# Performance work log

Measured on AMD Instinct MI355X. Metric: run time of the kernel, lower is better.

The kernel has to match this reference:

```python
import jax, jax.numpy as jnp
from jax import lax
import numpy as np

S, D, L, H, C = 128, 3, 16, 512, 10
B, T = 32, 16384


def setup_inputs() -> dict:
    key = jax.random.key(0)
    ks = jax.random.split(key, 6)
    x = jax.random.normal(ks[0], (B, D, T), dtype=jnp.float32)
    shapelets = jax.random.normal(ks[1], (S, 1, D, L), dtype=jnp.float32)  # OIHW, one per shapelet
    W1 = jax.random.normal(ks[2], (H, S), dtype=jnp.float32) * (1.0 / np.sqrt(S))
    b1 = jnp.zeros((H,), dtype=jnp.float32)
    W2 = jax.random.normal(ks[3], (C, H), dtype=jnp.float32) * (1.0 / np.sqrt(H))
    b2 = jnp.zeros((C,), dtype=jnp.float32)
    return {"x": x, "shapelets": shapelets, "W1": W1, "b1": b1, "W2": W2, "b2": b2}


def reference(x, shapelets, W1, b1, W2, b2):
    # x: [B, D, T] -> [B, 1, D, T]; kernels slide only over time (full-height conv).
    x4 = x[:, None, :, :]
    dn = ("NCHW", "OIHW", "NCHW")
    ones_k = jnp.ones((1, 1, shapelets.shape[2], shapelets.shape[3]), dtype=x.dtype)
    # ||window||^2 per sliding window: [B, 1, 1, Tout]
    window_square = lax.conv_general_dilated(x4 * x4, ones_k, (1, 1), "VALID", dimension_numbers=dn)
    # all cross-correlations in one grouped conv: [B, S, 1, Tout]
    cross_corr = lax.conv_general_dilated(x4, shapelets, (1, 1), "VALID", dimension_numbers=dn)
    shapelet_square = jnp.sum(shapelets * shapelets, axis=(1, 2, 3))  # [S]
    # squared distance per (shapelet, window), min-reduced over windows
    dist = window_square + shapelet_square[None, :, None, None] - 2.0 * cross_corr  # [B, S, 1, Tout]
    distance = jnp.min(dist, axis=(2, 3))  # [B, S]
    h = jax.nn.relu(distance @ W1.T + b1)
    classification = h @ W2.T + b2
    return (distance, classification)
```

## Files before the change

kernel.cpp:

```cpp
#include <hip/hip_runtime.h>

#define Bn 32
#define Tn 16384
#define Ln 16
#define Sn 128
#define Hn 512
#define Cn 10
#define Kn 48
#define TOUT 16369
#define CH 1024
#define NCH 16
#define XBP 8224

typedef short  s16x8  __attribute__((ext_vector_type(8)));
typedef float  f32x16 __attribute__((ext_vector_type(16)));

static __device__ __forceinline__ unsigned short f2bf(float f) {
    union { float f; unsigned int u; } v; v.f = f;
    unsigned int r = v.u + 0x7FFF + ((v.u >> 16) & 1);
    return (unsigned short)(r >> 16);
}
static __device__ __forceinline__ float bf2f(unsigned short b) {
    union { unsigned int u; float f; } v; v.u = ((unsigned int)b) << 16;
    return v.f;
}
static __device__ __forceinline__ unsigned int pk(float a, float b) {
    return (unsigned int)f2bf(a) | ((unsigned int)f2bf(b) << 16);
}
static __device__ __forceinline__ unsigned int pk2(unsigned short a, unsigned short b) {
    return (unsigned int)a | ((unsigned int)b << 16);
}
static __device__ __forceinline__ s16x8 mk_a(unsigned int d0, unsigned int d1,
                                             unsigned int d2, unsigned int d3) {
    union { unsigned int u[4]; s16x8 v; } t;
    t.u[0] = d0; t.u[1] = d1; t.u[2] = d2; t.u[3] = d3;
    return t.v;
}
static __device__ __forceinline__ s16x8 mk_a4(uint4 t) {
    union { uint4 u; s16x8 v; } c; c.u = t; return c.v;
}

__global__ __launch_bounds__(256) void prep_kernel(const float* __restrict__ x,
                                                   const float* __restrict__ sh,
                                                   const float* __restrict__ b2,
                                                   unsigned int* __restrict__ shb,
                                                   float* __restrict__ shsq_g,
                                                   float* __restrict__ wsqT,
                                                   unsigned int* __restrict__ xbf,
                                                   float* __restrict__ out) {
    const int tid = threadIdx.x;
    if (blockIdx.x == 0) {
        if (tid < 128) {
            const float4* r4 = (const float4*)(sh + tid * Kn);
            float v[48]; float q = 0.f;
            #pragma unroll
            for (int c = 0; c < 12; ++c) {
                const float4 t = r4[c];
                v[4*c] = t.x; v[4*c+1] = t.y; v[4*c+2] = t.z; v[4*c+3] = t.w;
                q = fmaf(t.x, t.x, q); q = fmaf(t.y, t.y, q);
                q = fmaf(t.z, t.z, q); q = fmaf(t.w, t.w, q);
            }
            shsq_g[tid] = q;
            uint4* dst = (uint4*)(shb + tid * 24);
            #pragma unroll
            for (int c = 0; c < 6; ++c) {
                uint4 o;
                o.x = pk(-2.f*v[8*c  ], -2.f*v[8*c+1]);
                o.y = pk(-2.f*v[8*c+2], -2.f*v[8*c+3]);
                o.z = pk(-2.f*v[8*c+4], -2.f*v[8*c+5]);
                o.w = pk(-2.f*v[8*c+6], -2.f*v[8*c+7]);
                dst[c] = o;
            }
        } else if (tid < 224) {
            const int r = tid - 128;
            uint4* d = (uint4*)(xbf + r * XBP + 8192);
            const uint4 z = {0u, 0u, 0u, 0u};
            #pragma unroll
            for (int q = 0; q < 8; ++q) d[q] = z;
        } else {
            const int k0 = (tid - 224) * 10;
            #pragma unroll
            for (int c = 0; c < Cn; ++c) out[Bn * Sn + k0 + c] = b2[c];
        }
        return;
    }
    const int bid = blockIdx.x - 1;
    const int b   = bid >> 4;
    const int t0  = ((bid & 15) << 10) + 4 * tid;
    float q[4] = {0.f, 0.f, 0.f, 0.f};
    #pragma unroll
    for (int ch = 0; ch < 3; ++ch) {
        const float* xs = x + (b * 3 + ch) * Tn + t0;
        float wv[20];
        if (t0 + 20 <= Tn) {
            const float4* x4 = (const float4*)xs;
            #pragma unroll
            for (int c = 0; c < 5; ++c) {
                const float4 t = x4[c];
                wv[4*c] = t.x; wv[4*c+1] = t.y; wv[4*c+2] = t.z; wv[4*c+3] = t.w;
            }
        } else {
            #pragma unroll
            for (int k = 0; k < 20; ++k) wv[k] = (t0 + k < Tn) ? xs[k] : 0.f;
        }
        float s = 0.f;
        #pragma unroll
        for (int l = 0; l < 16; ++l) s = fmaf(wv[l], wv[l], s);
        q[0] += s;
        #pragma unroll
        for (int j = 1; j < 4; ++j) {
            s = s - wv[j-1]*wv[j-1] + wv[j+15]*wv[j+15];
            q[j] += s;
        }
        uint2 o = { pk(wv[0], wv[1]), pk(wv[2], wv[3]) };
        *(uint2*)(xbf + (b * 3 + ch) * XBP + (t0 >> 1)) = o;
    }
    const int r0 = t0 & 15, col = t0 >> 4;
    float* wrow = wsqT + b * 16384 + col;
    #pragma unroll
    for (int c = 0; c < 4; ++c)
        wrow[(r0 + c) * 1024] = (t0 + c >= TOUT) ? 1e30f : q[c];
}

__global__ __launch_bounds__(256, 3) void dist_kernel(const unsigned int* __restrict__ shb,
                                                      const float* __restrict__ shsq_g,
                                                      const float* __restrict__ wsqT,
                                                      const unsigned int* __restrict__ xbf,
                                                      float* __restrict__ partial) {
    __shared__ float wavemin[4 * 64];

    const int tid   = threadIdx.x;
    const int b     = blockIdx.x >> 5;
    const int rem   = blockIdx.x & 31;
    const int chunk = rem >> 1;
    const int half  = rem & 1;
    const int tb    = chunk * CH;
    const int lane  = tid & 63;
    const int w     = tid >> 6;
    const int n     = lane & 31;
    const int h     = lane >> 5;

    s16x8 bfr[3][2], b4[2];
    #pragma unroll
    for (int st = 0; st < 2; ++st) {
        const int s = half * 64 + st * 32 + n;
        const uint4* base = (const uint4*)(shb + s * 24);
        #pragma unroll
        for (int kk = 0; kk < 3; ++kk) {
            const uint4 t = base[kk * 2 + h];
            bfr[kk][st] = mk_a(t.x, t.y, t.z, t.w);
        }
        const float q = shsq_g[s];
        const unsigned short qh = f2bf(q);
        const unsigned short ql = f2bf(q - bf2f(qh));
        b4[st] = h ? mk_a(0u, 0u, 0u, 0u)
                   : mk_a(0x3F803F80u, pk2(qh, ql), 0u, 0u);
    }

    unsigned int u[3][8];
    {
        const int D0 = (tb >> 1) + 4 * (w & 1) + ((w >> 1) << 8) + 8 * n + 4 * h;
        #pragma unroll
        for (int ch = 0; ch < 3; ++ch) {
            const unsigned int* xr = xbf + (b * 3 + ch) * XBP + D0;
            const uint4 lo = *(const uint4*)(xr);
            const uint4 hi = *(const uint4*)(xr + 4);
            u[ch][0] = lo.x; u[ch][1] = lo.y; u[ch][2] = lo.z; u[ch][3] = lo.w;
            u[ch][4] = hi.x; u[ch][5] = hi.y; u[ch][6] = hi.z; u[ch][7] = hi.w;
        }
    }

    float mcol[2] = {1e30f, 1e30f};
    const f32x16 zero16 = {0.f, 0.f, 0.f, 0.f, 0.f, 0.f, 0.f, 0.f,
                           0.f, 0.f, 0.f, 0.f, 0.f, 0.f, 0.f, 0.f};
    const int   base_t = 8 * (w & 1) + ((w >> 1) << 9);
    const float* wbase = wsqT + b * 16384 + (tb >> 4) + n;

    #pragma unroll
    for (int rr = 0; rr < 8; ++rr) {
        const int i = base_t + rr;
        s16x8 a[3];
        #pragma unroll
        for (int ch = 0; ch < 3; ++ch) {
            if ((rr & 1) == 0) {
                a[ch] = mk_a(u[ch][rr/2], u[ch][rr/2+1], u[ch][rr/2+2], u[ch][rr/2+3]);
            } else {
                unsigned int d[4];
                #pragma unroll
                for (int k = 0; k < 4; ++k)
                    d[k] = (u[ch][rr/2 + k] >> 16) | (u[ch][rr/2 + k + 1] << 16);
                a[ch] = mk_a(d[0], d[1], d[2], d[3]);
            }
        }
        const float wv = wbase[(i & 15) * 1024 + ((i >> 9) << 5)];
        const unsigned short wh = f2bf(wv);
        const unsigned short wl = f2bf(wv - bf2f(wh));
        const s16x8 a4 = h ? mk_a(0u, 0u, 0u, 0u)
                           : mk_a(pk2(wh, wl), 0x3F803F80u, 0u, 0u);

        #pragma unroll
        for (int st = 0; st < 2; ++st) {
            f32x16 acc;
            acc = __builtin_amdgcn_mfma_f32_32x32x16_bf16(a[0], bfr[0][st], zero16, 0, 0, 0);
            acc = __builtin_amdgcn_mfma_f32_32x32x16_bf16(a[1], bfr[1][st], acc, 0, 0, 0);
            acc = __builtin_amdgcn_mfma_f32_32x32x16_bf16(a[2], bfr[2][st], acc, 0, 0, 0);
            acc = __builtin_amdgcn_mfma_f32_32x32x16_bf16(a4,   b4[st],    acc, 0, 0, 0);
            #pragma unroll
            for (int reg = 0; reg < 16; reg += 2)
                mcol[st] = fminf(fminf(mcol[st], acc[reg]), acc[reg + 1]);
        }
    }

    #pragma unroll
    for (int st = 0; st < 2; ++st) {
        float mm = mcol[st];
        mm = fminf(mm, __shfl_xor(mm, 32, 64));
        if (h == 0) wavemin[w * 64 + st * 32 + n] = mm;
    }
    __syncthreads();
    if (tid < 64) {
        const float mm = fminf(fminf(wavemin[tid], wavemin[64 + tid]),
                               fminf(wavemin[128 + tid], wavemin[192 + tid]));
        partial[(b * NCH + chunk) * Sn + half * 64 + tid] = mm;
    }
}

__global__ __launch_bounds__(512) void mlp_kernel(const float* __restrict__ partial,
                                                  const float* __restrict__ W1,
                                                  const float* __restrict__ b1,
                                                  const float* __restrict__ W2,
                                                  float* __restrict__ out) {
    __shared__ float pmin[4][Sn];
    __shared__ float db[Sn];
    __shared__ float hb[128];
    __shared__ float part[Cn][32];
    const int b = blockIdx.x >> 2, g = blockIdx.x & 3, tid = threadIdx.x;

    {
        const int s = tid & 127, cg = tid >> 7;
        const float* pp = partial + (b * NCH + cg * 4) * Sn + s;
        float m = pp[0];
        #pragma unroll
        for (int c = 1; c < 4; ++c) m = fminf(m, pp[c * Sn]);
        pmin[cg][s] = m;
    }
    __syncthreads();
    if (tid < Sn) {
        const float m = fminf(fminf(pmin[0][tid], pmin[1][tid]),
                              fminf(pmin[2][tid], pmin[3][tid]));
        db[tid] = m;
        if (g == 0) out[b * Sn + tid] = m;
    }
    __syncthreads();

    if (tid < 128) {
        const int hrow = g * 128 + tid;
        float a = b1[hrow];
        const float4* w1r = (const float4*)(W1 + hrow * Sn);
        const float4* dbv = (const float4*)db;
        #pragma unroll
        for (int i = 0; i < Sn / 4; ++i) {
            const float4 wv = w1r[i];
            const float4 dv = dbv[i];
            a = fmaf(dv.x, wv.x, a); a = fmaf(dv.y, wv.y, a);
            a = fmaf(dv.z, wv.z, a); a = fmaf(dv.w, wv.w, a);
        }
        hb[tid] = fmaxf(a, 0.0f);
    }
    __syncthreads();

    if (tid < Cn * 32) {
        const int c = tid >> 5, p = tid & 31;
        float acc = 0.f;
        #pragma unroll
        for (int k = 0; k < 4; ++k)
            acc = fmaf(hb[p + 32 * k], W2[c * Hn + g * 128 + p + 32 * k], acc);
        part[c][p] = acc;
    }
    __syncthreads();
    if (tid < Cn) {
        float acc = 0.f;
        #pragma unroll
        for (int p = 0; p < 32; ++p) acc += part[tid][p];
        atomicAdd(&out[Bn * Sn + b * Cn + tid], acc);
    }
}

extern "C" void kernel_launch(void* const* d_in, const int* in_sizes, int n_in,
                              void* d_out, int out_size, void* d_ws, size_t ws_size,
                              hipStream_t stream) {
    const float* x  = (const float*)d_in[0];
    const float* sh = (const float*)d_in[1];
    const float* W1 = (const float*)d_in[2];
    const float* b1 = (const float*)d_in[3];
    const float* W2 = (const float*)d_in[4];
    const float* b2 = (const float*)d_in[5];
    float* out = (float*)d_out;

    char* wsb = (char*)d_ws;
    float*        partial = (float*)wsb;
    unsigned int* shb     = (unsigned int*)(wsb + 262144);
    float*        shsq_g  = (float*)(wsb + 274432);
    float*        wsqT    = (float*)(wsb + 278528);
    unsigned int* xbf     = (unsigned int*)(wsb + 2375680);

    prep_kernel<<<513, 256, 0, stream>>>(x, sh, b2, shb, shsq_g, wsqT, xbf, out);
    dist_kernel<<<Bn * NCH * 2, 256, 0, stream>>>(shb, shsq_g, wsqT, xbf, partial);
    mlp_kernel<<<Bn * 4, 512, 0, stream>>>(partial, W1, b1, W2, out);
}
```

Measured before the change: 97.78 us.

## Fuse prep kernel into distance kernel and drop MLP atomics

Removes the separate prep kernel. The distance kernel now reads fp32 x and the shapelets directly, converts them to bf16, and computes the sliding window squared norms and shapelet norms in registers. This cuts one launch and the round trip through the bf16/transposed workspace buffers, at the cost of redundant shapelet conversion per block and extra per-thread arithmetic. The MLP kernel now runs one block per batch over all 512 hidden units, adding b2 itself and writing the output directly instead of using atomicAdd.

```diff
diff --git a/kernel.cpp b/kernel.cpp
--- a/kernel.cpp
+++ b/kernel.cpp
@@ -10,7 +10,6 @@
 #define TOUT 16369
 #define CH 1024
 #define NCH 16
-#define XBP 8224
 
 typedef short  s16x8  __attribute__((ext_vector_type(8)));
 typedef float  f32x16 __attribute__((ext_vector_type(16)));
@@ -36,96 +35,9 @@
     t.u[0] = d0; t.u[1] = d1; t.u[2] = d2; t.u[3] = d3;
     return t.v;
 }
-static __device__ __forceinline__ s16x8 mk_a4(uint4 t) {
-    union { uint4 u; s16x8 v; } c; c.u = t; return c.v;
-}
-
-__global__ __launch_bounds__(256) void prep_kernel(const float* __restrict__ x,
-                                                   const float* __restrict__ sh,
-                                                   const float* __restrict__ b2,
-                                                   unsigned int* __restrict__ shb,
-                                                   float* __restrict__ shsq_g,
-                                                   float* __restrict__ wsqT,
-                                                   unsigned int* __restrict__ xbf,
-                                                   float* __restrict__ out) {
-    const int tid = threadIdx.x;
-    if (blockIdx.x == 0) {
-        if (tid < 128) {
-            const float4* r4 = (const float4*)(sh + tid * Kn);
-            float v[48]; float q = 0.f;
-            #pragma unroll
-            for (int c = 0; c < 12; ++c) {
-                const float4 t = r4[c];
-                v[4*c] = t.x; v[4*c+1] = t.y; v[4*c+2] = t.z; v[4*c+3] = t.w;
-                q = fmaf(t.x, t.x, q); q = fmaf(t.y, t.y, q);
-                q = fmaf(t.z, t.z, q); q = fmaf(t.w, t.w, q);
-            }
-            shsq_g[tid] = q;
-            uint4* dst = (uint4*)(shb + tid * 24);
-            #pragma unroll
-            for (int c = 0; c < 6; ++c) {
-                uint4 o;
-                o.x = pk(-2.f*v[8*c  ], -2.f*v[8*c+1]);
-                o.y = pk(-2.f*v[8*c+2], -2.f*v[8*c+3]);
-                o.z = pk(-2.f*v[8*c+4], -2.f*v[8*c+5]);
-                o.w = pk(-2.f*v[8*c+6], -2.f*v[8*c+7]);
-                dst[c] = o;
-            }
-        } else if (tid < 224) {
-            const int r = tid - 128;
-            uint4* d = (uint4*)(xbf + r * XBP + 8192);
-            const uint4 z = {0u, 0u, 0u, 0u};
-            #pragma unroll
-            for (int q = 0; q < 8; ++q) d[q] = z;
-        } else {
-            const int k0 = (tid - 224) * 10;
-            #pragma unroll
-            for (int c = 0; c < Cn; ++c) out[Bn * Sn + k0 + c] = b2[c];
-        }
-        return;
-    }
-    const int bid = blockIdx.x - 1;
-    const int b   = bid >> 4;
-    const int t0  = ((bid & 15) << 10) + 4 * tid;
-    float q[4] = {0.f, 0.f, 0.f, 0.f};
-    #pragma unroll
-    for (int ch = 0; ch < 3; ++ch) {
-        const float* xs = x + (b * 3 + ch) * Tn + t0;
-        float wv[20];
-        if (t0 + 20 <= Tn) {
-            const float4* x4 = (const float4*)xs;
-            #pragma unroll
-            for (int c = 0; c < 5; ++c) {
-                const float4 t = x4[c];
-                wv[4*c] = t.x; wv[4*c+1] = t.y; wv[4*c+2] = t.z; wv[4*c+3] = t.w;
-            }
-        } else {
-            #pragma unroll
-            for (int k = 0; k < 20; ++k) wv[k] = (t0 + k < Tn) ? xs[k] : 0.f;
-        }
-        float s = 0.f;
-        #pragma unroll
-        for (int l = 0; l < 16; ++l) s = fmaf(wv[l], wv[l], s);
-        q[0] += s;
-        #pragma unroll
-        for (int j = 1; j < 4; ++j) {
-            s = s - wv[j-1]*wv[j-1] + wv[j+15]*wv[j+15];
-            q[j] += s;
-        }
-        uint2 o = { pk(wv[0], wv[1]), pk(wv[2], wv[3]) };
-        *(uint2*)(xbf + (b * 3 + ch) * XBP + (t0 >> 1)) = o;
-    }
-    const int r0 = t0 & 15, col = t0 >> 4;
-    float* wrow = wsqT + b * 16384 + col;
-    #pragma unroll
-    for (int c = 0; c < 4; ++c)
-        wrow[(r0 + c) * 1024] = (t0 + c >= TOUT) ? 1e30f : q[c];
-}
-
-__global__ __launch_bounds__(256, 3) void dist_kernel(const unsigned int* __restrict__ shb,
-                                                      const float* __restrict__ shsq_g,
-                                                      const float* __restrict__ wsqT,
-                                                      const unsigned int* __restrict__ xbf,
+
+__global__ __launch_bounds__(256, 3) void dist_kernel(const float* __restrict__ x,
+                                                      const float* __restrict__ sh,
                                                       float* __restrict__ partial) {
     __shared__ float wavemin[4 * 64];
 
@@ -144,41 +56,79 @@
     #pragma unroll
     for (int st = 0; st < 2; ++st) {
         const int s = half * 64 + st * 32 + n;
-        const uint4* base = (const uint4*)(shb + s * 24);
+        const float4* row4 = (const float4*)(sh + s * Kn);
+        float q = 0.f;
         #pragma unroll
         for (int kk = 0; kk < 3; ++kk) {
-            const uint4 t = base[kk * 2 + h];
-            bfr[kk][st] = mk_a(t.x, t.y, t.z, t.w);
-        }
-        const float q = shsq_g[s];
+            const float4 v0 = row4[kk * 4 + 0];
+            const float4 v1 = row4[kk * 4 + 1];
+            const float4 v2 = row4[kk * 4 + 2];
+            const float4 v3 = row4[kk * 4 + 3];
+            q = fmaf(v0.x, v0.x, q); q = fmaf(v0.y, v0.y, q);
+            q = fmaf(v0.z, v0.z, q); q = fmaf(v0.w, v0.w, q);
+            q = fmaf(v1.x, v1.x, q); q = fmaf(v1.y, v1.y, q);
+            q = fmaf(v1.z, v1.z, q); q = fmaf(v1.w, v1.w, q);
+            q = fmaf(v2.x, v2.x, q); q = fmaf(v2.y, v2.y, q);
+            q = fmaf(v2.z, v2.z, q); q = fmaf(v2.w, v2.w, q);
+            q = fmaf(v3.x, v3.x, q); q = fmaf(v3.y, v3.y, q);
+            q = fmaf(v3.z, v3.z, q); q = fmaf(v3.w, v3.w, q);
+            const float4 pa = h ? v2 : v0;
+            const float4 pb = h ? v3 : v1;
+            bfr[kk][st] = mk_a(pk(-2.f * pa.x, -2.f * pa.y),
+                               pk(-2.f * pa.z, -2.f * pa.w),
+                               pk(-2.f * pb.x, -2.f * pb.y),
+                               pk(-2.f * pb.z, -2.f * pb.w));
+        }
         const unsigned short qh = f2bf(q);
         const unsigned short ql = f2bf(q - bf2f(qh));
         b4[st] = h ? mk_a(0u, 0u, 0u, 0u)
                    : mk_a(0x3F803F80u, pk2(qh, ql), 0u, 0u);
     }
 
+    const int t0 = tb + 8 * (w & 1) + ((w >> 1) << 9) + 16 * n + 8 * h;
     unsigned int u[3][8];
-    {
-        const int D0 = (tb >> 1) + 4 * (w & 1) + ((w >> 1) << 8) + 8 * n + 4 * h;
-        #pragma unroll
-        for (int ch = 0; ch < 3; ++ch) {
-            const unsigned int* xr = xbf + (b * 3 + ch) * XBP + D0;
-            const uint4 lo = *(const uint4*)(xr);
-            const uint4 hi = *(const uint4*)(xr + 4);
-            u[ch][0] = lo.x; u[ch][1] = lo.y; u[ch][2] = lo.z; u[ch][3] = lo.w;
-            u[ch][4] = hi.x; u[ch][5] = hi.y; u[ch][6] = hi.z; u[ch][7] = hi.w;
-        }
+    float q8[8] = {0.f, 0.f, 0.f, 0.f, 0.f, 0.f, 0.f, 0.f};
+    #pragma unroll
+    for (int ch = 0; ch < 3; ++ch) {
+        const float* xs = x + (b * 3 + ch) * Tn + t0;
+        float wv[24];
+        if (t0 + 24 <= Tn) {
+            const float4* x4 = (const float4*)xs;
+            #pragma unroll
+            for (int c = 0; c < 6; ++c) {
+                const float4 t = x4[c];
+                wv[4*c] = t.x; wv[4*c+1] = t.y; wv[4*c+2] = t.z; wv[4*c+3] = t.w;
+            }
+        } else {
+            #pragma unroll
+            for (int k = 0; k < 24; ++k) wv[k] = (t0 + k < Tn) ? xs[k] : 0.f;
+        }
+        #pragma unroll
+        for (int e = 0; e < 8; ++e) u[ch][e] = pk(wv[2*e], wv[2*e+1]);
+        float s = 0.f;
+        #pragma unroll
+        for (int l = 0; l < 16; ++l) s = fmaf(wv[l], wv[l], s);
+        q8[0] += s;
+        #pragma unroll
+        for (int j = 1; j < 8; ++j) {
+            s = s - wv[j-1] * wv[j-1] + wv[j+15] * wv[j+15];
+            q8[j] += s;
+        }
+    }
+    unsigned int wqp[8];
+    #pragma unroll
+    for (int rr = 0; rr < 8; ++rr) {
+        const float qv = (t0 + rr >= TOUT) ? 1e30f : q8[rr];
+        const unsigned short wh_ = f2bf(qv);
+        const unsigned short wl_ = f2bf(qv - bf2f(wh_));
+        wqp[rr] = pk2(wh_, wl_);
     }
 
     float mcol[2] = {1e30f, 1e30f};
     const f32x16 zero16 = {0.f, 0.f, 0.f, 0.f, 0.f, 0.f, 0.f, 0.f,
                            0.f, 0.f, 0.f, 0.f, 0.f, 0.f, 0.f, 0.f};
-    const int   base_t = 8 * (w & 1) + ((w >> 1) << 9);
-    const float* wbase = wsqT + b * 16384 + (tb >> 4) + n;
-
     #pragma unroll
     for (int rr = 0; rr < 8; ++rr) {
-        const int i = base_t + rr;
         s16x8 a[3];
         #pragma unroll
         for (int ch = 0; ch < 3; ++ch) {
@@ -192,11 +142,8 @@
                 a[ch] = mk_a(d[0], d[1], d[2], d[3]);
             }
         }
-        const float wv = wbase[(i & 15) * 1024 + ((i >> 9) << 5)];
-        const unsigned short wh = f2bf(wv);
-        const unsigned short wl = f2bf(wv - bf2f(wh));
         const s16x8 a4 = h ? mk_a(0u, 0u, 0u, 0u)
-                           : mk_a(pk2(wh, wl), 0x3F803F80u, 0u, 0u);
+                           : mk_a(wqp[rr], 0x3F803F80u, 0u, 0u);
 
         #pragma unroll
         for (int st = 0; st < 2; ++st) {
@@ -229,60 +176,58 @@
                                                   const float* __restrict__ W1,
                                                   const float* __restrict__ b1,
                                                   const float* __restrict__ W2,
+                                                  const float* __restrict__ b2,
                                                   float* __restrict__ out) {
     __shared__ float pmin[4][Sn];
     __shared__ float db[Sn];
-    __shared__ float hb[128];
+    __shared__ float hb[Hn];
     __shared__ float part[Cn][32];
-    const int b = blockIdx.x >> 2, g = blockIdx.x & 3, tid = threadIdx.x;
+    const int b = blockIdx.x, tid = threadIdx.x;
 
     {
-        const int s = tid & 127, cg = tid >> 7;
-        const float* pp = partial + (b * NCH + cg * 4) * Sn + s;
+        const int s = tid & 127, g = tid >> 7;
+        const float* pp = partial + (b * NCH + g * 4) * Sn + s;
         float m = pp[0];
         #pragma unroll
         for (int c = 1; c < 4; ++c) m = fminf(m, pp[c * Sn]);
-        pmin[cg][s] = m;
+        pmin[g][s] = m;
     }
     __syncthreads();
     if (tid < Sn) {
         const float m = fminf(fminf(pmin[0][tid], pmin[1][tid]),
                               fminf(pmin[2][tid], pmin[3][tid]));
         db[tid] = m;
-        if (g == 0) out[b * Sn + tid] = m;
-    }
-    __syncthreads();
-
-    if (tid < 128) {
-        const int hrow = g * 128 + tid;
-        float a = b1[hrow];
-        const float4* w1r = (const float4*)(W1 + hrow * Sn);
-        const float4* dbv = (const float4*)db;
-        #pragma unroll
-        for (int i = 0; i < Sn / 4; ++i) {
-            const float4 wv = w1r[i];
-            const float4 dv = dbv[i];
-            a = fmaf(dv.x, wv.x, a); a = fmaf(dv.y, wv.y, a);
-            a = fmaf(dv.z, wv.z, a); a = fmaf(dv.w, wv.w, a);
-        }
-        hb[tid] = fmaxf(a, 0.0f);
-    }
+        out[b * Sn + tid] = m;
+    }
+    __syncthreads();
+
+    float a = b1[tid];
+    const float4* w1r = (const float4*)(W1 + tid * Sn);
+    const float4* dbv = (const float4*)db;
+    #pragma unroll
+    for (int i = 0; i < Sn / 4; ++i) {
+        const float4 wv = w1r[i];
+        const float4 dv = dbv[i];
+        a = fmaf(dv.x, wv.x, a); a = fmaf(dv.y, wv.y, a);
+        a = fmaf(dv.z, wv.z, a); a = fmaf(dv.w, wv.w, a);
+    }
+    hb[tid] = fmaxf(a, 0.0f);
     __syncthreads();
 
     if (tid < Cn * 32) {
         const int c = tid >> 5, p = tid & 31;
         float acc = 0.f;
         #pragma unroll
-        for (int k = 0; k < 4; ++k)
-            acc = fmaf(hb[p + 32 * k], W2[c * Hn + g * 128 + p + 32 * k], acc);
+        for (int i = 0; i < Hn / 32; ++i)
+            acc = fmaf(hb[p + 32 * i], W2[c * Hn + p + 32 * i], acc);
         part[c][p] = acc;
     }
     __syncthreads();
     if (tid < Cn) {
-        float acc = 0.f;
+        float acc = b2[tid];
         #pragma unroll
         for (int p = 0; p < 32; ++p) acc += part[tid][p];
-        atomicAdd(&out[Bn * Sn + b * Cn + tid], acc);
+        out[Bn * Sn + b * Cn + tid] = acc;
     }
 }
 
@@ -296,15 +241,8 @@
     const float* W2 = (const float*)d_in[4];
     const float* b2 = (const float*)d_in[5];
     float* out = (float*)d_out;
-
-    char* wsb = (char*)d_ws;
-    float*        partial = (float*)wsb;
-    unsigned int* shb     = (unsigned int*)(wsb + 262144);
-    float*        shsq_g  = (float*)(wsb + 274432);
-    float*        wsqT    = (float*)(wsb + 278528);
-    unsigned int* xbf     = (unsigned int*)(wsb + 2375680);
-
-    prep_kernel<<<513, 256, 0, stream>>>(x, sh, b2, shb, shsq_g, wsqT, xbf, out);
-    dist_kernel<<<Bn * NCH * 2, 256, 0, stream>>>(shb, shsq_g, wsqT, xbf, partial);
-    mlp_kernel<<<Bn * 4, 512, 0, stream>>>(partial, W1, b1, W2, out);
-}
+    float* partial = (float*)d_ws;
+
+    dist_kernel<<<Bn * NCH * 2, 256, 0, stream>>>(x, sh, partial);
+    mlp_kernel<<<Bn, 512, 0, stream>>>(partial, W1, b1, W2, b2, out);
+}
```

After: 124.1 us. 1.27x slower.
